# Kernel optimization log

Hardware: AMD Instinct MI355X
Metric: run time of the kernel (lower is better)

## Reference

```python
import jax, jax.numpy as jnp
import numpy as np

HEADS = 8
SR = 8


def _layernorm(x, g, b):
    m = jnp.mean(x, axis=-1, keepdims=True)
    v = jnp.var(x, axis=-1, keepdims=True)
    return (x - m) / jnp.sqrt(v + 1e-5) * g + b


def _sr_conv(x, w, b):
    # x: [B,C,H,W], w: [C,C,SR,SR] (OIHW), stride=SR, no padding
    y = jax.lax.conv_general_dilated(x, w, (SR, SR), 'VALID',
                                     dimension_numbers=('NCHW', 'OIHW', 'NCHW'))
    return y + b[None, :, None, None]


def _attn(xq, xkv, qw, kvw, pw, pb, srw, srb, lng, lnb, H, W):
    # xq: [B,N,C] queries (also residual); xkv: [B,N,C] key/value source
    B, N, C = xq.shape
    hd = C // HEADS
    scale = hd ** -0.5
    q = (xq @ qw.T).reshape(B, N, HEADS, hd).transpose(0, 2, 1, 3)  # [B,h,N,d]
    x_ = xkv.transpose(0, 2, 1).reshape(B, C, H, W)
    x_ = _sr_conv(x_, srw, srb).reshape(B, C, -1).transpose(0, 2, 1)  # [B,Nkv,C]
    x_ = _layernorm(x_, lng, lnb)
    kv = (x_ @ kvw.T).reshape(B, -1, 2, HEADS, hd).transpose(2, 0, 3, 1, 4)
    k, v = kv[0], kv[1]  # [B,h,Nkv,d]
    a = jax.nn.softmax(jnp.einsum('bhnd,bhmd->bhnm', q, k) * scale, axis=-1)
    o = jnp.einsum('bhnm,bhmd->bhnd', a, v).transpose(0, 2, 1, 3).reshape(B, N, C)
    return (o + xq) @ pw.T + pb


def _forward(x1, x2,
             sa1_qw, sa1_kvw, sa1_pw, sa1_pb, sa1_srw, sa1_srb, sa1_lng, sa1_lnb,
             ca12_qw, ca12_kvw, ca12_pw, ca12_pb, ca12_srw, ca12_srb, ca12_lng, ca12_lnb,
             sa2_qw, sa2_kvw, sa2_pw, sa2_pb, sa2_srw, sa2_srb, sa2_lng, sa2_lnb,
             ca21_qw, ca21_kvw, ca21_pw, ca21_pb, ca21_srw, ca21_srb, ca21_lng, ca21_lnb,
             pw, pb):
    B, C, H, W = x1.shape
    x1f = x1.reshape(B, C, H * W).transpose(0, 2, 1)
    x2f = x2.reshape(B, C, H * W).transpose(0, 2, 1)
    a = _attn(x1f, x1f, sa1_qw, sa1_kvw, sa1_pw, sa1_pb, sa1_srw, sa1_srb, sa1_lng, sa1_lnb, H, W)
    # CrossAttention(x2_flat, x1_self): queries/residual from x2, kv from x1_self
    b = _attn(x2f, a, ca12_qw, ca12_kvw, ca12_pw, ca12_pb, ca12_srw, ca12_srb, ca12_lng, ca12_lnb, H, W)
    c = _attn(b, b, sa2_qw, sa2_kvw, sa2_pw, sa2_pb, sa2_srw, sa2_srb, sa2_lng, sa2_lnb, H, W)
    d = _attn(a, c, ca21_qw, ca21_kvw, ca21_pw, ca21_pb, ca21_srw, ca21_srb, ca21_lng, ca21_lnb, H, W)
    fuse = d @ pw.T + pb
    return fuse.transpose(0, 2, 1).reshape(B, C, H, W)


def setup_inputs() -> dict:
    key = jax.random.key(0)
    B, C, H, W = 2, 64, 112, 112
    keys = iter(jax.random.split(key, 64))
    nrm = lambda shape, s=0.02: jax.random.normal(next(keys), shape, jnp.float32) * s
    d = {
        'x1': jax.random.normal(next(keys), (B, C, H, W), jnp.float32),
        'x2': jax.random.normal(next(keys), (B, C, H, W), jnp.float32),
    }
    conv_std = float(np.sqrt(2.0 / (SR * SR * C)))
    for p in ['sa1', 'ca12', 'sa2', 'ca21']:
        d[p + '_qw'] = nrm((C, C))
        d[p + '_kvw'] = nrm((2 * C, C))
        d[p + '_pw'] = nrm((C, C))
        d[p + '_pb'] = jnp.zeros((C,), jnp.float32)
        d[p + '_srw'] = nrm((C, C, SR, SR), conv_std)
        d[p + '_srb'] = jnp.zeros((C,), jnp.float32)
        d[p + '_lng'] = jnp.ones((C,), jnp.float32)
        d[p + '_lnb'] = jnp.zeros((C,), jnp.float32)
    d['pw'] = nrm((C, C))
    d['pb'] = jnp.zeros((C,), jnp.float32)
    return d


def reference(x1, x2,
              sa1_qw, sa1_kvw, sa1_pw, sa1_pb, sa1_srw, sa1_srb, sa1_lng, sa1_lnb,
              ca12_qw, ca12_kvw, ca12_pw, ca12_pb, ca12_srw, ca12_srb, ca12_lng, ca12_lnb,
              sa2_qw, sa2_kvw, sa2_pw, sa2_pb, sa2_srw, sa2_srb, sa2_lng, sa2_lnb,
              ca21_qw, ca21_kvw, ca21_pw, ca21_pb, ca21_srw, ca21_srb, ca21_lng, ca21_lnb,
              pw, pb):
    return _forward(x1, x2,
                    sa1_qw, sa1_kvw, sa1_pw, sa1_pb, sa1_srw, sa1_srb, sa1_lng, sa1_lnb,
                    ca12_qw, ca12_kvw, ca12_pw, ca12_pb, ca12_srw, ca12_srb, ca12_lng, ca12_lnb,
                    sa2_qw, sa2_kvw, sa2_pw, sa2_pb, sa2_srw, sa2_srb, sa2_lng, sa2_lnb,
                    ca21_qw, ca21_kvw, ca21_pw, ca21_pb, ca21_srw, ca21_srb, ca21_lng, ca21_lnb,
                    pw, pb)
```

## Files before the change

### kernel.cpp

```cpp
#include <hip/hip_runtime.h>
#include <hip/hip_bf16.h>

#define NPIX 12544
#define NKV 196
#define CCH 64

typedef _Float16 half2_t __attribute__((ext_vector_type(2)));
typedef _Float16 half4_t __attribute__((ext_vector_type(4)));
typedef float float4_t __attribute__((ext_vector_type(4)));
typedef __fp16 fp16v2_t __attribute__((ext_vector_type(2)));

#if defined(__has_builtin)
#if __has_builtin(__builtin_amdgcn_fdot2)
#define HAVE_FDOT2 1
#endif
#if __has_builtin(__builtin_amdgcn_cvt_pkrtz)
#define HAVE_PKRTZ 1
#endif
#if __has_builtin(__builtin_amdgcn_exp2f)
#define HAVE_EXP2 1
#endif
#if __has_builtin(__builtin_amdgcn_mfma_f32_16x16x16f16)
#define HAVE_MFMA16 1
#endif
#endif

__device__ __forceinline__ float dot2acc(half2_t a, half2_t b, float c) {
#ifdef HAVE_FDOT2
  return __builtin_amdgcn_fdot2(a, b, c, false);
#else
  return c + (float)a.x * (float)b.x + (float)a.y * (float)b.y;
#endif
}

__device__ __forceinline__ half2_t pack2(float a, float b) {
#ifdef HAVE_PKRTZ
  union { fp16v2_t r; half2_t h; } u;
  u.r = __builtin_amdgcn_cvt_pkrtz(a, b);
  return u.h;
#else
  half2_t v; v.x = (_Float16)a; v.y = (_Float16)b; return v;
#endif
}

__device__ __forceinline__ half2_t as_h2(uint u) {
  union { uint v; half2_t h; } c; c.v = u; return c.h;
}
__device__ __forceinline__ uint h2u(half2_t h) {
  union { half2_t h; uint v; } c; c.h = h; return c.v;
}
__device__ __forceinline__ float fexp2(float x) {
#ifdef HAVE_EXP2
  return __builtin_amdgcn_exp2f(x);
#else
  return exp2f(x);
#endif
}

__device__ __forceinline__ float4_t mfma16(half4_t a, half4_t b, float4_t c) {
#ifdef HAVE_MFMA16
  return __builtin_amdgcn_mfma_f32_16x16x16f16(a, b, c, 0, 0, 0);
#else
  asm volatile("v_mfma_f32_16x16x16_f16 %0, %1, %2, %0" : "+v"(c) : "v"(a), "v"(b));
  return c;
#endif
}

union U2H4 { uint2 u; half4_t h; };

#define QSCALE 0.5100974012336431f

__global__ __launch_bounds__(256) void k_prep(
    const float* __restrict__ x1, const float* __restrict__ x2,
    float* __restrict__ x1f, float* __restrict__ x2f,
    const float* __restrict__ s0, const float* __restrict__ s1,
    const float* __restrict__ s2, const float* __restrict__ s3,
    float* __restrict__ wt,
    const float* __restrict__ fpw, const float* __restrict__ fpb,
    const float* __restrict__ pw4, const float* __restrict__ pb4,
    const float* __restrict__ pw0, const float* __restrict__ pw1,
    const float* __restrict__ pw2,
    uint* __restrict__ pwh, float* __restrict__ pbc) {
  __shared__ float smem[2 * 64 * 65 + 64];
  int blk = blockIdx.x, t = threadIdx.x;
  float (*tile)[65] = (float(*)[65])smem;
  if (blk < 784) {
    int tensor = blk / 392; int rem = blk - tensor * 392;
    int b = rem / 196; int t64 = rem % 196; int n0 = t64 * 64;
    const float* src = tensor ? x2 : x1;
    float* dst = tensor ? x2f : x1f;
    for (int i = 0; i < 16; ++i) {
      int c = i * 4 + (t >> 6);
      int n = t & 63;
      tile[c][n] = src[(b * 64 + c) * NPIX + n0 + n];
    }
    __syncthreads();
    for (int i = 0; i < 16; ++i) {
      int n = i * 4 + (t >> 6);
      int c = t & 63;
      dst[(b * NPIX + n0 + n) * 64 + c] = tile[c][n];
    }
  } else if (blk < 1040) {
    int id = blk - 784; int a = id >> 6; int ci = id & 63;
    const float* s = (a == 0) ? s0 : (a == 1) ? s1 : (a == 2) ? s2 : s3;
    float* d = wt + a * 262144;
    for (int i = 0; i < 16; ++i) {
      int co = i * 4 + (t >> 6);
      int ij = t & 63;
      tile[co][ij] = s[co * 4096 + ci * 64 + ij];
    }
    __syncthreads();
    for (int i = 0; i < 16; ++i) {
      int ij = i * 4 + (t >> 6);
      int co = t & 63;
      d[(ij * 64 + ci) * 64 + co] = tile[co][ij];
    }
  } else if (blk == 1040) {
    float (*A)[65] = (float(*)[65])smem;
    float (*B)[65] = (float(*)[65])(smem + 4160);
    float* bb = smem + 8320;
    for (int i = 0; i < 16; ++i) {
      int idx = i * 256 + t;
      A[idx >> 6][idx & 63] = fpw[idx];
      B[idx >> 6][idx & 63] = pw4[idx];
    }
    if (t < 64) bb[t] = pb4[t];
    __syncthreads();
    int i = t >> 2, jq = t & 3;
    float acc[16];
#pragma unroll
    for (int jj = 0; jj < 16; ++jj) acc[jj] = 0.f;
    for (int k = 0; k < 64; ++k) {
      float a = A[i][k];
#pragma unroll
      for (int jj = 0; jj < 16; ++jj) acc[jj] += a * B[k][jq * 16 + jj];
    }
#pragma unroll
    for (int m = 0; m < 8; ++m)
      pwh[3 * 2048 + (jq * 8 + m) * 64 + i] = h2u(pack2(acc[2 * m], acc[2 * m + 1]));
    if (t < 64) {
      float s = fpb[t];
      for (int k = 0; k < 64; ++k) s += A[t][k] * bb[k];
      pbc[t] = s;
    }
  } else {
    int a = blk - 1041;
    const float* pw = (a == 0) ? pw0 : (a == 1) ? pw1 : pw2;
    for (int i = 0; i < 8; ++i) {
      int idx = i * 256 + t;
      int co = idx & 63, c2 = idx >> 6;
      float2 wv = *(const float2*)(pw + co * 64 + c2 * 2);
      pwh[a * 2048 + c2 * 64 + co] = h2u(pack2(wv.x, wv.y));
    }
  }
}

__global__ __launch_bounds__(256) void k_conv(
    const float* __restrict__ xf, const float* __restrict__ wt,
    float* __restrict__ part) {
  __shared__ __align__(16) float act[8 * 8 * 72];
  __shared__ float red[16][8][65];
  int g = blockIdx.x % 49, s = blockIdx.x / 49;
  int t = threadIdx.x;
  for (int q = 0; q < 5; ++q) {
    int fi = q * 256 + t;
    if (fi < 1152) {
      int row = fi / 18, pos = fi % 18;
      if (pos < 16) {
        int pix = row >> 3, ijl = row & 7;
        int ij = s * 8 + ijl, ii = ij >> 3, jj = ij & 7;
        int p = g * 8 + pix, b = p / 196, pi = p % 196;
        int py = pi / 14, px = pi % 14;
        *(float4*)&act[row * 72 + pos * 4] =
            *(const float4*)(xf + (size_t)(b * NPIX + (8 * py + ii) * 112 + 8 * px + jj) * 64 + pos * 4);
      }
    }
  }
  __syncthreads();
  int coq = t & 15, kp = t >> 4;
  int ijl = kp >> 1, ci0 = (kp & 1) * 32;
  float acc[8][4];
#pragma unroll
  for (int p = 0; p < 8; ++p)
#pragma unroll
    for (int c = 0; c < 4; ++c) acc[p][c] = 0.f;
  const float* wb = wt + ((s * 8 + ijl) * 64 + ci0) * 64 + coq * 4;
  const float* ab = act + ijl * 72 + ci0;
  for (int kk = 0; kk < 32; ++kk) {
    float4 w4 = *(const float4*)(wb + kk * 64);
#pragma unroll
    for (int p = 0; p < 8; ++p) {
      float a = ab[p * 576 + kk];
      acc[p][0] += a * w4.x; acc[p][1] += a * w4.y;
      acc[p][2] += a * w4.z; acc[p][3] += a * w4.w;
    }
  }
#pragma unroll
  for (int p = 0; p < 8; ++p)
#pragma unroll
    for (int c = 0; c < 4; ++c) red[kp][p][coq * 4 + c] = acc[p][c];
  __syncthreads();
  for (int q = 0; q < 2; ++q) {
    int oi = t + q * 256;
    int pix = oi >> 6, co = oi & 63;
    float sum = 0.f;
#pragma unroll
    for (int k = 0; k < 16; ++k) sum += red[k][pix][co];
    int p = g * 8 + pix;
    part[(s * 392 + p) * 64 + co] = sum;
  }
}

__global__ __launch_bounds__(128) void k_lnkv(
    const float* __restrict__ part, const float* __restrict__ srb,
    const float* __restrict__ lng, const float* __restrict__ lnb,
    const float* __restrict__ kvw,
    _Float16* __restrict__ kbuf, _Float16* __restrict__ vbuf) {
  __shared__ __align__(16) float yn[64];
  __shared__ __align__(16) float4 lkvw[16][128];
  int p = blockIdx.x, t = threadIdx.x;
  for (int i = 0; i < 64; ++i) {
    int idx = i * 128 + t;
    int co2 = idx >> 6, ci = idx & 63;
    ((float*)lkvw)[(ci >> 2) * 512 + co2 * 4 + (ci & 3)] = kvw[idx];
  }
  if (t < 64) {
    float y = 0.f;
    for (int s = 0; s < 8; ++s) y += part[(s * 392 + p) * 64 + t];
    y += srb[t];
    float s1 = y, s2 = y * y;
#pragma unroll
    for (int off = 32; off; off >>= 1) { s1 += __shfl_xor(s1, off); s2 += __shfl_xor(s2, off); }
    float mean = s1 * 0.015625f;
    float var = s2 * 0.015625f - mean * mean;
    float rs = rsqrtf(var + 1e-5f);
    yn[t] = (y - mean) * rs * lng[t] + lnb[t];
  }
  __syncthreads();
  float acc = 0.f;
#pragma unroll
  for (int c4 = 0; c4 < 16; ++c4) {
    float4 w4 = lkvw[c4][t];
    float4 y4 = *(const float4*)&yn[c4 * 4];
    acc += y4.x * w4.x + y4.y * w4.y + y4.z * w4.z + y4.w * w4.w;
  }
  int b = p / 196, pi = p % 196;
  int h = (t & 63) >> 3, d = t & 7;
  if (t < 64) kbuf[((b * 8 + h) * 196 + pi) * 8 + d] = (_Float16)acc;
  else        vbuf[((b * 8 + h) * 8 + d) * 196 + pi] = (_Float16)acc;
}

template <bool FINAL>
__global__ __launch_bounds__(512, 2) void k_score_out(
    const float* __restrict__ xqf, const float* __restrict__ qw,
    const _Float16* __restrict__ kbuf, const _Float16* __restrict__ vbuf,
    const uint* __restrict__ pwh, const float* __restrict__ pb,
    float* __restrict__ outp) {
  __shared__ __align__(16) uint sW[2048];
  __shared__ __align__(16) uint sX[64 * 33];
  __shared__ __align__(16) uint lq[8 * 64 * 4];
  __shared__ __align__(16) uint lo[64 * 34];
  int blk = blockIdx.x;
  int b = blk / 196, tileb = blk % 196;
  int t = threadIdx.x;
  int h = t >> 6, l = t & 63;
  int r15 = l & 15, g = l >> 4;
  for (int i = t; i < 2048; i += 512) {
    int co = i & 63, c2 = i >> 6;
    float2 wv = *(const float2*)(qw + co * 64 + c2 * 2);
    sW[c2 * 64 + co] = h2u(pack2(wv.x * QSCALE, wv.y * QSCALE));
  }
  for (int i = t; i < 2048; i += 512) {
    int rr = i >> 5, c2 = i & 31;
    float2 v = *(const float2*)(xqf + ((size_t)b * NPIX + (size_t)tileb * 64 + rr) * 64 + c2 * 2);
    sX[rr * 33 + c2] = h2u(pack2(v.x, v.y));
  }
  __syncthreads();
  {
    float q8[8];
#pragma unroll
    for (int j = 0; j < 8; ++j) q8[j] = 0.f;
#pragma unroll
    for (int c2 = 0; c2 < 32; ++c2) {
      half2_t xv = as_h2(sX[l * 33 + c2]);
      uint4 w0 = *(const uint4*)&sW[c2 * 64 + h * 8];
      uint4 w1 = *(const uint4*)&sW[c2 * 64 + h * 8 + 4];
      q8[0] = dot2acc(xv, as_h2(w0.x), q8[0]);
      q8[1] = dot2acc(xv, as_h2(w0.y), q8[1]);
      q8[2] = dot2acc(xv, as_h2(w0.z), q8[2]);
      q8[3] = dot2acc(xv, as_h2(w0.w), q8[3]);
      q8[4] = dot2acc(xv, as_h2(w1.x), q8[4]);
      q8[5] = dot2acc(xv, as_h2(w1.y), q8[5]);
      q8[6] = dot2acc(xv, as_h2(w1.z), q8[6]);
      q8[7] = dot2acc(xv, as_h2(w1.w), q8[7]);
    }
    uint4 qp;
    qp.x = h2u(pack2(q8[0], q8[1])); qp.y = h2u(pack2(q8[2], q8[3]));
    qp.z = h2u(pack2(q8[4], q8[5])); qp.w = h2u(pack2(q8[6], q8[7]));
    *(uint4*)&lq[(h * 64 + l) * 4] = qp;
  }
  __syncthreads();
  int bh = b * 8 + h;
  half4_t kf[13], vf[13];
#pragma unroll
  for (int tt = 0; tt < 13; ++tt) {
    int m = tt * 16 + r15;
    if (g < 2 && m < 196) {
      U2H4 u; u.u = *(const uint2*)(kbuf + ((size_t)bh * 196 + m) * 8 + 4 * g);
      kf[tt] = u.h;
    } else {
      kf[tt] = (half4_t)(_Float16)0.f;
    }
    int mv = tt * 16 + 4 * g;
    if (r15 < 8 && mv + 3 < 196) {
      U2H4 u; u.u = *(const uint2*)(vbuf + ((size_t)bh * 8 + r15) * 196 + mv);
      vf[tt] = u.h;
    } else {
      vf[tt] = (half4_t)(_Float16)0.f;
    }
  }
#pragma unroll 1
  for (int rt = 0; rt < 4; ++rt) {
    int rbase = rt * 16;
    half4_t qf;
    if (g < 2) {
      U2H4 u; u.u = *(const uint2*)((const _Float16*)nullptr);
      u.u = *(const uint2*)&lq[(h * 64 + rbase + r15) * 4 + 2 * g];
      qf = u.h;
    } else {
      qf = (half4_t)(_Float16)0.f;
    }
    float4_t sacc[13];
#pragma unroll
    for (int tt = 0; tt < 13; ++tt) {
      float4_t z = {0.f, 0.f, 0.f, 0.f};
      sacc[tt] = mfma16(kf[tt], qf, z);
    }
    float ssum = 0.f;
    half4_t pbf[13];
#pragma unroll
    for (int tt = 0; tt < 13; ++tt) {
      float e0, e1, e2, e3;
      if (tt == 12 && g > 0) {
        e0 = e1 = e2 = e3 = 0.f;
      } else {
        e0 = fexp2(sacc[tt][0]); e1 = fexp2(sacc[tt][1]);
        e2 = fexp2(sacc[tt][2]); e3 = fexp2(sacc[tt][3]);
      }
      ssum += (e0 + e1) + (e2 + e3);
      half2_t p01 = pack2(e0, e1), p23 = pack2(e2, e3);
      half4_t pv; pv.x = p01.x; pv.y = p01.y; pv.z = p23.x; pv.w = p23.y;
      pbf[tt] = pv;
    }
    ssum += __shfl_xor(ssum, 16);
    ssum += __shfl_xor(ssum, 32);
    float rl = 1.f / ssum;
    float4_t oacc = {0.f, 0.f, 0.f, 0.f};
#pragma unroll
    for (int tt = 0; tt < 13; ++tt) oacc = mfma16(vf[tt], pbf[tt], oacc);
    if (g < 2) {
      uint2 ov;
      ov.x = h2u(pack2(oacc[0] * rl, oacc[1] * rl));
      ov.y = h2u(pack2(oacc[2] * rl, oacc[3] * rl));
      *(uint2*)&lo[(rbase + r15) * 34 + h * 4 + 2 * g] = ov;
    }
  }
  __syncthreads();
  for (int i = t; i < 2048; i += 512) sW[i] = pwh[i];
  __syncthreads();
  int r2 = t >> 3, cq = t & 7;
  size_t gr2 = (size_t)b * NPIX + (size_t)tileb * 64 + r2;
  float acc[8];
#pragma unroll
  for (int k = 0; k < 8; ++k) acc[k] = pb[cq * 8 + k];
#pragma unroll
  for (int c2 = 0; c2 < 32; ++c2) {
    half2_t sv = as_h2(lo[r2 * 34 + c2]) + as_h2(sX[r2 * 33 + c2]);
    uint4 w0 = *(const uint4*)&sW[c2 * 64 + cq * 8];
    uint4 w1 = *(const uint4*)&sW[c2 * 64 + cq * 8 + 4];
    acc[0] = dot2acc(sv, as_h2(w0.x), acc[0]);
    acc[1] = dot2acc(sv, as_h2(w0.y), acc[1]);
    acc[2] = dot2acc(sv, as_h2(w0.z), acc[2]);
    acc[3] = dot2acc(sv, as_h2(w0.w), acc[3]);
    acc[4] = dot2acc(sv, as_h2(w1.x), acc[4]);
    acc[5] = dot2acc(sv, as_h2(w1.y), acc[5]);
    acc[6] = dot2acc(sv, as_h2(w1.z), acc[6]);
    acc[7] = dot2acc(sv, as_h2(w1.w), acc[7]);
  }
  if (!FINAL) {
    float4 v0, v1;
    v0.x = acc[0]; v0.y = acc[1]; v0.z = acc[2]; v0.w = acc[3];
    v1.x = acc[4]; v1.y = acc[5]; v1.z = acc[6]; v1.w = acc[7];
    float* orow = outp + gr2 * 64 + cq * 8;
    *(float4*)orow = v0;
    *(float4*)(orow + 4) = v1;
  } else {
    __syncthreads();
    uint2 p0, p1;
    p0.x = h2u(pack2(acc[0], acc[1])); p0.y = h2u(pack2(acc[2], acc[3]));
    p1.x = h2u(pack2(acc[4], acc[5])); p1.y = h2u(pack2(acc[6], acc[7]));
    *(uint2*)&lo[r2 * 34 + cq * 4] = p0;
    *(uint2*)&lo[r2 * 34 + cq * 4 + 2] = p1;
    __syncthreads();
    for (int i = t; i < 4096; i += 512) {
      int c = i >> 6, rr = i & 63;
      half2_t pr = as_h2(lo[rr * 34 + (c >> 1)]);
      float val = (c & 1) ? (float)pr.y : (float)pr.x;
      outp[((size_t)(b * 64 + c)) * NPIX + (size_t)tileb * 64 + rr] = val;
    }
  }
}

extern "C" void kernel_launch(void* const* d_in, const int* in_sizes, int n_in,
                              void* d_out, int out_size, void* d_ws, size_t ws_size,
                              hipStream_t stream) {
  const float* x1 = (const float*)d_in[0];
  const float* x2 = (const float*)d_in[1];
  const float *qw[4], *kvw[4], *pwv[4], *pbv[4], *srw[4], *srb[4], *lng[4], *lnb[4];
  for (int i = 0; i < 4; ++i) {
    const int base = 2 + i * 8;
    qw[i]  = (const float*)d_in[base + 0];
    kvw[i] = (const float*)d_in[base + 1];
    pwv[i] = (const float*)d_in[base + 2];
    pbv[i] = (const float*)d_in[base + 3];
    srw[i] = (const float*)d_in[base + 4];
    srb[i] = (const float*)d_in[base + 5];
    lng[i] = (const float*)d_in[base + 6];
    lnb[i] = (const float*)d_in[base + 7];
  }
  const float* fpw = (const float*)d_in[34];
  const float* fpb = (const float*)d_in[35];
  float* out = (float*)d_out;

  char* ws = (char*)d_ws;
  const size_t SZ = (size_t)2 * NPIX * 64 * 4;
  float* slot0 = (float*)(ws);
  float* slot1 = (float*)(ws + SZ);
  float* slot2 = (float*)(ws + 2 * SZ);
  size_t off = 3 * SZ;
  float* wt    = (float*)(ws + off); off += 4u * 1048576;
  float* part  = (float*)(ws + off); off += 802816;
  _Float16* kbuf = (_Float16*)(ws + off); off += 50176;
  _Float16* vbuf = (_Float16*)(ws + off); off += 50176;
  uint* pwh    = (uint*)(ws + off); off += 4 * 2048 * 4;
  float* pbc   = (float*)(ws + off); off += 256;

  float* xf1 = slot0; float* xf2 = slot1;
  float* abuf = slot2; float* bbuf = slot0; float* cbuf = slot1;

  k_prep<<<1044, 256, 0, stream>>>(x1, x2, xf1, xf2,
                                   srw[0], srw[1], srw[2], srw[3], wt,
                                   fpw, fpb, pwv[3], pbv[3],
                                   pwv[0], pwv[1], pwv[2], pwh, pbc);

  const float* xqs[4] = {xf1, xf2, bbuf, abuf};
  const float* kvs[4] = {xf1, abuf, bbuf, cbuf};
  float* outs[3]      = {abuf, bbuf, cbuf};
  for (int i = 0; i < 4; ++i) {
    k_conv<<<392, 256, 0, stream>>>(kvs[i], wt + i * 262144, part);
    k_lnkv<<<392, 128, 0, stream>>>(part, srb[i], lng[i], lnb[i], kvw[i], kbuf, vbuf);
    if (i < 3)
      k_score_out<false><<<392, 512, 0, stream>>>(xqs[i], qw[i], kbuf, vbuf,
                                                  pwh + i * 2048, pbv[i], outs[i]);
    else
      k_score_out<true><<<392, 512, 0, stream>>>(xqs[3], qw[3], kbuf, vbuf,
                                                 pwh + 3 * 2048, pbc, out);
  }
}
```

Baseline: 146.8 us.

## Fuse SR conv with LayerNorm+KV projection using fp16 packed weights

Merges the strided conv and the LayerNorm/KV-projection kernels into one kernel per output pixel, removing the partial-sum buffer and one launch per stage. The conv weights are pre-transposed into packed fp16 pairs and activations are converted to fp16 in shared memory, so the conv uses fdot2 instead of fp32 FMAs. Each block now streams the full 64x64x64 weight set itself (no split over kernel positions across blocks), which raises per-block global weight traffic and lowers precision of the conv inputs.

```diff
diff --git a/kernel.cpp b/kernel.cpp
--- a/kernel.cpp
+++ b/kernel.cpp
@@ -75,7 +75,7 @@
     float* __restrict__ x1f, float* __restrict__ x2f,
     const float* __restrict__ s0, const float* __restrict__ s1,
     const float* __restrict__ s2, const float* __restrict__ s3,
-    float* __restrict__ wt,
+    uint* __restrict__ wth,
     const float* __restrict__ fpw, const float* __restrict__ fpb,
     const float* __restrict__ pw4, const float* __restrict__ pb4,
     const float* __restrict__ pw0, const float* __restrict__ pw1,
@@ -101,19 +101,18 @@
       dst[(b * NPIX + n0 + n) * 64 + c] = tile[c][n];
     }
   } else if (blk < 1040) {
-    int id = blk - 784; int a = id >> 6; int ci = id & 63;
+    int id = blk - 784; int a = id >> 6; int co = id & 63;
     const float* s = (a == 0) ? s0 : (a == 1) ? s1 : (a == 2) ? s2 : s3;
-    float* d = wt + a * 262144;
-    for (int i = 0; i < 16; ++i) {
-      int co = i * 4 + (t >> 6);
-      int ij = t & 63;
-      tile[co][ij] = s[co * 4096 + ci * 64 + ij];
-    }
+    float* cw = smem;
+    for (int i = 0; i < 16; ++i)
+      cw[i * 256 + t] = s[co * 4096 + i * 256 + t];
     __syncthreads();
-    for (int i = 0; i < 16; ++i) {
-      int ij = i * 4 + (t >> 6);
-      int co = t & 63;
-      d[(ij * 64 + ci) * 64 + co] = tile[co][ij];
+    uint* wdst = wth + (size_t)a * 131072;
+    for (int q = 0; q < 8; ++q) {
+      int oi = q * 256 + t;
+      int ij = oi >> 5, ci2 = oi & 31;
+      wdst[((size_t)ij * 64 + co) * 32 + ci2] =
+          h2u(pack2(cw[(2 * ci2) * 64 + ij], cw[(2 * ci2 + 1) * 64 + ij]));
     }
   } else if (blk == 1040) {
     float (*A)[65] = (float(*)[65])smem;
@@ -155,78 +154,52 @@
   }
 }
 
-__global__ __launch_bounds__(256) void k_conv(
-    const float* __restrict__ xf, const float* __restrict__ wt,
-    float* __restrict__ part) {
-  __shared__ __align__(16) float act[8 * 8 * 72];
-  __shared__ float red[16][8][65];
-  int g = blockIdx.x % 49, s = blockIdx.x / 49;
-  int t = threadIdx.x;
-  for (int q = 0; q < 5; ++q) {
-    int fi = q * 256 + t;
-    if (fi < 1152) {
-      int row = fi / 18, pos = fi % 18;
-      if (pos < 16) {
-        int pix = row >> 3, ijl = row & 7;
-        int ij = s * 8 + ijl, ii = ij >> 3, jj = ij & 7;
-        int p = g * 8 + pix, b = p / 196, pi = p % 196;
-        int py = pi / 14, px = pi % 14;
-        *(float4*)&act[row * 72 + pos * 4] =
-            *(const float4*)(xf + (size_t)(b * NPIX + (8 * py + ii) * 112 + 8 * px + jj) * 64 + pos * 4);
-      }
-    }
-  }
-  __syncthreads();
-  int coq = t & 15, kp = t >> 4;
-  int ijl = kp >> 1, ci0 = (kp & 1) * 32;
-  float acc[8][4];
-#pragma unroll
-  for (int p = 0; p < 8; ++p)
-#pragma unroll
-    for (int c = 0; c < 4; ++c) acc[p][c] = 0.f;
-  const float* wb = wt + ((s * 8 + ijl) * 64 + ci0) * 64 + coq * 4;
-  const float* ab = act + ijl * 72 + ci0;
-  for (int kk = 0; kk < 32; ++kk) {
-    float4 w4 = *(const float4*)(wb + kk * 64);
-#pragma unroll
-    for (int p = 0; p < 8; ++p) {
-      float a = ab[p * 576 + kk];
-      acc[p][0] += a * w4.x; acc[p][1] += a * w4.y;
-      acc[p][2] += a * w4.z; acc[p][3] += a * w4.w;
-    }
-  }
-#pragma unroll
-  for (int p = 0; p < 8; ++p)
-#pragma unroll
-    for (int c = 0; c < 4; ++c) red[kp][p][coq * 4 + c] = acc[p][c];
-  __syncthreads();
+__global__ __launch_bounds__(512) void k_convlnkv(
+    const float* __restrict__ xf, const uint* __restrict__ wth,
+    const float* __restrict__ srb, const float* __restrict__ lng,
+    const float* __restrict__ lnb, const float* __restrict__ kvw,
+    _Float16* __restrict__ kbuf, _Float16* __restrict__ vbuf) {
+  __shared__ __align__(16) uint act16[64 * 32];
+  __shared__ float red[8][66];
+  __shared__ __align__(16) float yn[64];
+  __shared__ __align__(16) float lkvw[128 * 68];
+  int p = blockIdx.x, t = threadIdx.x;
+  int b = p / 196, pi = p % 196, py = pi / 14, px = pi % 14;
   for (int q = 0; q < 2; ++q) {
-    int oi = t + q * 256;
-    int pix = oi >> 6, co = oi & 63;
-    float sum = 0.f;
-#pragma unroll
-    for (int k = 0; k < 16; ++k) sum += red[k][pix][co];
-    int p = g * 8 + pix;
-    part[(s * 392 + p) * 64 + co] = sum;
-  }
-}
-
-__global__ __launch_bounds__(128) void k_lnkv(
-    const float* __restrict__ part, const float* __restrict__ srb,
-    const float* __restrict__ lng, const float* __restrict__ lnb,
-    const float* __restrict__ kvw,
-    _Float16* __restrict__ kbuf, _Float16* __restrict__ vbuf) {
-  __shared__ __align__(16) float yn[64];
-  __shared__ __align__(16) float4 lkvw[16][128];
-  int p = blockIdx.x, t = threadIdx.x;
-  for (int i = 0; i < 64; ++i) {
-    int idx = i * 128 + t;
-    int co2 = idx >> 6, ci = idx & 63;
-    ((float*)lkvw)[(ci >> 2) * 512 + co2 * 4 + (ci & 3)] = kvw[idx];
-  }
+    int fi = q * 512 + t;
+    int ij = fi >> 4, pos = fi & 15;
+    int ii = ij >> 3, jj = ij & 7;
+    float4 v = *(const float4*)(xf + ((size_t)(b * NPIX + (8 * py + ii) * 112 + 8 * px + jj) * 64 + pos * 4));
+    uint2 pk; pk.x = h2u(pack2(v.x, v.y)); pk.y = h2u(pack2(v.z, v.w));
+    *(uint2*)&act16[ij * 32 + pos * 2] = pk;
+  }
+  for (int i = 0; i < 16; ++i) {
+    int idx = i * 512 + t;
+    lkvw[(idx >> 6) * 68 + (idx & 63)] = kvw[idx];
+  }
+  __syncthreads();
+  int co = t & 63, g8 = t >> 6;
+  float acc = 0.f;
+  for (int ij8 = 0; ij8 < 8; ++ij8) {
+    int ij = g8 * 8 + ij8;
+    const uint4* wrow = (const uint4*)(wth + ((size_t)ij * 64 + co) * 32);
+    const uint4* arow = (const uint4*)(act16 + ij * 32);
+#pragma unroll
+    for (int u = 0; u < 8; ++u) {
+      uint4 w = wrow[u];
+      uint4 a = arow[u];
+      acc = dot2acc(as_h2(a.x), as_h2(w.x), acc);
+      acc = dot2acc(as_h2(a.y), as_h2(w.y), acc);
+      acc = dot2acc(as_h2(a.z), as_h2(w.z), acc);
+      acc = dot2acc(as_h2(a.w), as_h2(w.w), acc);
+    }
+  }
+  red[g8][co] = acc;
+  __syncthreads();
   if (t < 64) {
     float y = 0.f;
-    for (int s = 0; s < 8; ++s) y += part[(s * 392 + p) * 64 + t];
+#pragma unroll
+    for (int k = 0; k < 8; ++k) y += red[k][t];
     y += srb[t];
     float s1 = y, s2 = y * y;
 #pragma unroll
@@ -237,17 +210,23 @@
     yn[t] = (y - mean) * rs * lng[t] + lnb[t];
   }
   __syncthreads();
-  float acc = 0.f;
-#pragma unroll
-  for (int c4 = 0; c4 < 16; ++c4) {
-    float4 w4 = lkvw[c4][t];
-    float4 y4 = *(const float4*)&yn[c4 * 4];
-    acc += y4.x * w4.x + y4.y * w4.y + y4.z * w4.z + y4.w * w4.w;
-  }
-  int b = p / 196, pi = p % 196;
-  int h = (t & 63) >> 3, d = t & 7;
-  if (t < 64) kbuf[((b * 8 + h) * 196 + pi) * 8 + d] = (_Float16)acc;
-  else        vbuf[((b * 8 + h) * 8 + d) * 196 + pi] = (_Float16)acc;
+  if (t < 128) {
+    int o = t;
+    float a2 = 0.f;
+#pragma unroll
+    for (int c4 = 0; c4 < 16; ++c4) {
+      float4 w4 = *(const float4*)&lkvw[o * 68 + c4 * 4];
+      float4 y4 = *(const float4*)&yn[c4 * 4];
+      a2 += y4.x * w4.x + y4.y * w4.y + y4.z * w4.z + y4.w * w4.w;
+    }
+    if (o < 64) {
+      int h = o >> 3, d = o & 7;
+      kbuf[((b * 8 + h) * 196 + pi) * 8 + d] = (_Float16)a2;
+    } else {
+      int oo = o - 64, h = oo >> 3, d = oo & 7;
+      vbuf[((b * 8 + h) * 8 + d) * 196 + pi] = (_Float16)a2;
+    }
+  }
 }
 
 template <bool FINAL>
@@ -324,7 +303,7 @@
     int rbase = rt * 16;
     half4_t qf;
     if (g < 2) {
-      U2H4 u; u.u = *(const uint2*)((const _Float16*)nullptr);
+      U2H4 u;
       u.u = *(const uint2*)&lq[(h * 64 + rbase + r15) * 4 + 2 * g];
       qf = u.h;
     } else {
@@ -438,8 +417,7 @@
   float* slot1 = (float*)(ws + SZ);
   float* slot2 = (float*)(ws + 2 * SZ);
   size_t off = 3 * SZ;
-  float* wt    = (float*)(ws + off); off += 4u * 1048576;
-  float* part  = (float*)(ws + off); off += 802816;
+  uint* wth    = (uint*)(ws + off); off += (size_t)4 * 131072 * 4;
   _Float16* kbuf = (_Float16*)(ws + off); off += 50176;
   _Float16* vbuf = (_Float16*)(ws + off); off += 50176;
   uint* pwh    = (uint*)(ws + off); off += 4 * 2048 * 4;
@@ -449,7 +427,7 @@
   float* abuf = slot2; float* bbuf = slot0; float* cbuf = slot1;
 
   k_prep<<<1044, 256, 0, stream>>>(x1, x2, xf1, xf2,
-                                   srw[0], srw[1], srw[2], srw[3], wt,
+                                   srw[0], srw[1], srw[2], srw[3], wth,
                                    fpw, fpb, pwv[3], pbv[3],
                                    pwv[0], pwv[1], pwv[2], pwh, pbc);
 
@@ -457,8 +435,8 @@
   const float* kvs[4] = {xf1, abuf, bbuf, cbuf};
   float* outs[3]      = {abuf, bbuf, cbuf};
   for (int i = 0; i < 4; ++i) {
-    k_conv<<<392, 256, 0, stream>>>(kvs[i], wt + i * 262144, part);
-    k_lnkv<<<392, 128, 0, stream>>>(part, srb[i], lng[i], lnb[i], kvw[i], kbuf, vbuf);
+    k_convlnkv<<<392, 512, 0, stream>>>(kvs[i], wth + (size_t)i * 131072,
+                                        srb[i], lng[i], lnb[i], kvw[i], kbuf, vbuf);
     if (i < 3)
       k_score_out<false><<<392, 512, 0, stream>>>(xqs[i], qw[i], kbuf, vbuf,
                                                   pwh + i * 2048, pbv[i], outs[i]);
```

Measured after the change: 251.1 us. 71.0% more time.

## Halve row tile of score/output kernel to 32 rows and double grid size

Applied to the files above, without the earlier changes.

The fused attention-score/projection kernel now processes 32 query rows per block instead of 64, launching 784 blocks instead of 392 to fill more compute units on the 256-CU device. The Q projection splits the channel reduction across two half-waves and combines them with a cross-lane shuffle, and the output projection gives each thread 4 output channels instead of 8. The intent is better occupancy and load balance. The cost is that each block reloads the weight tiles and K/V fragments for half as many rows, doubling that redundant traffic.

```diff
diff --git a/kernel.cpp b/kernel.cpp
--- a/kernel.cpp
+++ b/kernel.cpp
@@ -257,11 +257,11 @@
     const uint* __restrict__ pwh, const float* __restrict__ pb,
     float* __restrict__ outp) {
   __shared__ __align__(16) uint sW[2048];
-  __shared__ __align__(16) uint sX[64 * 33];
-  __shared__ __align__(16) uint lq[8 * 64 * 4];
-  __shared__ __align__(16) uint lo[64 * 34];
+  __shared__ __align__(16) uint sX[32 * 33];
+  __shared__ __align__(16) uint lq[8 * 32 * 4];
+  __shared__ __align__(16) uint lo[32 * 34];
   int blk = blockIdx.x;
-  int b = blk / 196, tileb = blk % 196;
+  int b = blk / 392, tileb = blk % 392;
   int t = threadIdx.x;
   int h = t >> 6, l = t & 63;
   int r15 = l & 15, g = l >> 4;
@@ -270,19 +270,21 @@
     float2 wv = *(const float2*)(qw + co * 64 + c2 * 2);
     sW[c2 * 64 + co] = h2u(pack2(wv.x * QSCALE, wv.y * QSCALE));
   }
-  for (int i = t; i < 2048; i += 512) {
+  for (int i = t; i < 1024; i += 512) {
     int rr = i >> 5, c2 = i & 31;
-    float2 v = *(const float2*)(xqf + ((size_t)b * NPIX + (size_t)tileb * 64 + rr) * 64 + c2 * 2);
+    float2 v = *(const float2*)(xqf + ((size_t)b * NPIX + (size_t)tileb * 32 + rr) * 64 + c2 * 2);
     sX[rr * 33 + c2] = h2u(pack2(v.x, v.y));
   }
   __syncthreads();
   {
+    int r = l & 31, khalf = l >> 5;
     float q8[8];
 #pragma unroll
     for (int j = 0; j < 8; ++j) q8[j] = 0.f;
 #pragma unroll
-    for (int c2 = 0; c2 < 32; ++c2) {
-      half2_t xv = as_h2(sX[l * 33 + c2]);
+    for (int c2i = 0; c2i < 16; ++c2i) {
+      int c2 = khalf * 16 + c2i;
+      half2_t xv = as_h2(sX[r * 33 + c2]);
       uint4 w0 = *(const uint4*)&sW[c2 * 64 + h * 8];
       uint4 w1 = *(const uint4*)&sW[c2 * 64 + h * 8 + 4];
       q8[0] = dot2acc(xv, as_h2(w0.x), q8[0]);
@@ -294,10 +296,14 @@
       q8[6] = dot2acc(xv, as_h2(w1.z), q8[6]);
       q8[7] = dot2acc(xv, as_h2(w1.w), q8[7]);
     }
-    uint4 qp;
-    qp.x = h2u(pack2(q8[0], q8[1])); qp.y = h2u(pack2(q8[2], q8[3]));
-    qp.z = h2u(pack2(q8[4], q8[5])); qp.w = h2u(pack2(q8[6], q8[7]));
-    *(uint4*)&lq[(h * 64 + l) * 4] = qp;
+#pragma unroll
+    for (int j = 0; j < 8; ++j) q8[j] += __shfl_xor(q8[j], 32);
+    if (khalf == 0) {
+      uint4 qp;
+      qp.x = h2u(pack2(q8[0], q8[1])); qp.y = h2u(pack2(q8[2], q8[3]));
+      qp.z = h2u(pack2(q8[4], q8[5])); qp.w = h2u(pack2(q8[6], q8[7]));
+      *(uint4*)&lq[(h * 32 + r) * 4] = qp;
+    }
   }
   __syncthreads();
   int bh = b * 8 + h;
@@ -320,12 +326,12 @@
     }
   }
 #pragma unroll 1
-  for (int rt = 0; rt < 4; ++rt) {
+  for (int rt = 0; rt < 2; ++rt) {
     int rbase = rt * 16;
     half4_t qf;
     if (g < 2) {
-      U2H4 u; u.u = *(const uint2*)((const _Float16*)nullptr);
-      u.u = *(const uint2*)&lq[(h * 64 + rbase + r15) * 4 + 2 * g];
+      U2H4 u;
+      u.u = *(const uint2*)&lq[(h * 32 + rbase + r15) * 4 + 2 * g];
       qf = u.h;
     } else {
       qf = (half4_t)(_Float16)0.f;
@@ -368,45 +374,34 @@
   __syncthreads();
   for (int i = t; i < 2048; i += 512) sW[i] = pwh[i];
   __syncthreads();
-  int r2 = t >> 3, cq = t & 7;
-  size_t gr2 = (size_t)b * NPIX + (size_t)tileb * 64 + r2;
-  float acc[8];
-#pragma unroll
-  for (int k = 0; k < 8; ++k) acc[k] = pb[cq * 8 + k];
+  int r2 = t >> 4, cq = t & 15;
+  size_t gr2 = (size_t)b * NPIX + (size_t)tileb * 32 + r2;
+  float acc[4];
+#pragma unroll
+  for (int k = 0; k < 4; ++k) acc[k] = pb[cq * 4 + k];
 #pragma unroll
   for (int c2 = 0; c2 < 32; ++c2) {
     half2_t sv = as_h2(lo[r2 * 34 + c2]) + as_h2(sX[r2 * 33 + c2]);
-    uint4 w0 = *(const uint4*)&sW[c2 * 64 + cq * 8];
-    uint4 w1 = *(const uint4*)&sW[c2 * 64 + cq * 8 + 4];
-    acc[0] = dot2acc(sv, as_h2(w0.x), acc[0]);
-    acc[1] = dot2acc(sv, as_h2(w0.y), acc[1]);
-    acc[2] = dot2acc(sv, as_h2(w0.z), acc[2]);
-    acc[3] = dot2acc(sv, as_h2(w0.w), acc[3]);
-    acc[4] = dot2acc(sv, as_h2(w1.x), acc[4]);
-    acc[5] = dot2acc(sv, as_h2(w1.y), acc[5]);
-    acc[6] = dot2acc(sv, as_h2(w1.z), acc[6]);
-    acc[7] = dot2acc(sv, as_h2(w1.w), acc[7]);
+    uint4 w = *(const uint4*)&sW[c2 * 64 + cq * 4];
+    acc[0] = dot2acc(sv, as_h2(w.x), acc[0]);
+    acc[1] = dot2acc(sv, as_h2(w.y), acc[1]);
+    acc[2] = dot2acc(sv, as_h2(w.z), acc[2]);
+    acc[3] = dot2acc(sv, as_h2(w.w), acc[3]);
   }
   if (!FINAL) {
-    float4 v0, v1;
-    v0.x = acc[0]; v0.y = acc[1]; v0.z = acc[2]; v0.w = acc[3];
-    v1.x = acc[4]; v1.y = acc[5]; v1.z = acc[6]; v1.w = acc[7];
-    float* orow = outp + gr2 * 64 + cq * 8;
-    *(float4*)orow = v0;
-    *(float4*)(orow + 4) = v1;
+    float4 v;
+    v.x = acc[0]; v.y = acc[1]; v.z = acc[2]; v.w = acc[3];
+    *(float4*)(outp + gr2 * 64 + cq * 4) = v;
   } else {
     __syncthreads();
-    uint2 p0, p1;
-    p0.x = h2u(pack2(acc[0], acc[1])); p0.y = h2u(pack2(acc[2], acc[3]));
-    p1.x = h2u(pack2(acc[4], acc[5])); p1.y = h2u(pack2(acc[6], acc[7]));
-    *(uint2*)&lo[r2 * 34 + cq * 4] = p0;
-    *(uint2*)&lo[r2 * 34 + cq * 4 + 2] = p1;
+    lo[r2 * 34 + cq * 2] = h2u(pack2(acc[0], acc[1]));
+    lo[r2 * 34 + cq * 2 + 1] = h2u(pack2(acc[2], acc[3]));
     __syncthreads();
-    for (int i = t; i < 4096; i += 512) {
-      int c = i >> 6, rr = i & 63;
+    for (int i = t; i < 2048; i += 512) {
+      int c = i >> 5, rr = i & 31;
       half2_t pr = as_h2(lo[rr * 34 + (c >> 1)]);
       float val = (c & 1) ? (float)pr.y : (float)pr.x;
-      outp[((size_t)(b * 64 + c)) * NPIX + (size_t)tileb * 64 + rr] = val;
+      outp[((size_t)(b * 64 + c)) * NPIX + (size_t)tileb * 32 + rr] = val;
     }
   }
 }
@@ -460,10 +455,10 @@
     k_conv<<<392, 256, 0, stream>>>(kvs[i], wt + i * 262144, part);
     k_lnkv<<<392, 128, 0, stream>>>(part, srb[i], lng[i], lnb[i], kvw[i], kbuf, vbuf);
     if (i < 3)
-      k_score_out<false><<<392, 512, 0, stream>>>(xqs[i], qw[i], kbuf, vbuf,
+      k_score_out<false><<<784, 512, 0, stream>>>(xqs[i], qw[i], kbuf, vbuf,
                                                   pwh + i * 2048, pbv[i], outs[i]);
     else
-      k_score_out<true><<<392, 512, 0, stream>>>(xqs[3], qw[3], kbuf, vbuf,
+      k_score_out<true><<<784, 512, 0, stream>>>(xqs[3], qw[3], kbuf, vbuf,
                                                  pwh + 3 * 2048, pbc, out);
   }
 }
```

Measured after the change: 190.9 us. 30.0% more time.

## Compute Q projection with MFMA in-loop and preload projection weights early

Applied to the files above, without the earlier changes.

The per-thread fdot2 Q projection, which wrote to a shared `lq` buffer, is replaced by 16x16x16 MFMA ops computed per row tile inside the attention loop. Each wave-pair computes Q for 16 channels and uses a lane shuffle to hand the odd head its half. The output-projection weights are now loaded into an enlarged shared buffer at kernel start, which removes a later reload and barrier. This cuts ALU work and two syncs, at the cost of redundant MFMA work across paired waves, more shared memory for weights, and extra register pressure for the A fragments.

```diff
diff --git a/kernel.cpp b/kernel.cpp
--- a/kernel.cpp
+++ b/kernel.cpp
@@ -256,50 +256,36 @@
     const _Float16* __restrict__ kbuf, const _Float16* __restrict__ vbuf,
     const uint* __restrict__ pwh, const float* __restrict__ pb,
     float* __restrict__ outp) {
-  __shared__ __align__(16) uint sW[2048];
+  __shared__ __align__(16) uint sW[4096];
   __shared__ __align__(16) uint sX[64 * 33];
-  __shared__ __align__(16) uint lq[8 * 64 * 4];
   __shared__ __align__(16) uint lo[64 * 34];
   int blk = blockIdx.x;
   int b = blk / 196, tileb = blk % 196;
   int t = threadIdx.x;
   int h = t >> 6, l = t & 63;
   int r15 = l & 15, g = l >> 4;
+  int ht = h >> 1, odd = h & 1;
   for (int i = t; i < 2048; i += 512) {
     int co = i & 63, c2 = i >> 6;
     float2 wv = *(const float2*)(qw + co * 64 + c2 * 2);
     sW[c2 * 64 + co] = h2u(pack2(wv.x * QSCALE, wv.y * QSCALE));
   }
+  for (int i = t; i < 2048; i += 512) sW[2048 + i] = pwh[i];
   for (int i = t; i < 2048; i += 512) {
     int rr = i >> 5, c2 = i & 31;
     float2 v = *(const float2*)(xqf + ((size_t)b * NPIX + (size_t)tileb * 64 + rr) * 64 + c2 * 2);
     sX[rr * 33 + c2] = h2u(pack2(v.x, v.y));
   }
   __syncthreads();
-  {
-    float q8[8];
-#pragma unroll
-    for (int j = 0; j < 8; ++j) q8[j] = 0.f;
-#pragma unroll
-    for (int c2 = 0; c2 < 32; ++c2) {
-      half2_t xv = as_h2(sX[l * 33 + c2]);
-      uint4 w0 = *(const uint4*)&sW[c2 * 64 + h * 8];
-      uint4 w1 = *(const uint4*)&sW[c2 * 64 + h * 8 + 4];
-      q8[0] = dot2acc(xv, as_h2(w0.x), q8[0]);
-      q8[1] = dot2acc(xv, as_h2(w0.y), q8[1]);
-      q8[2] = dot2acc(xv, as_h2(w0.z), q8[2]);
-      q8[3] = dot2acc(xv, as_h2(w0.w), q8[3]);
-      q8[4] = dot2acc(xv, as_h2(w1.x), q8[4]);
-      q8[5] = dot2acc(xv, as_h2(w1.y), q8[5]);
-      q8[6] = dot2acc(xv, as_h2(w1.z), q8[6]);
-      q8[7] = dot2acc(xv, as_h2(w1.w), q8[7]);
-    }
-    uint4 qp;
-    qp.x = h2u(pack2(q8[0], q8[1])); qp.y = h2u(pack2(q8[2], q8[3]));
-    qp.z = h2u(pack2(q8[4], q8[5])); qp.w = h2u(pack2(q8[6], q8[7]));
-    *(uint4*)&lq[(h * 64 + l) * 4] = qp;
-  }
-  __syncthreads();
+  half4_t Aq[4];
+#pragma unroll
+  for (int ch = 0; ch < 4; ++ch) {
+    uint u0 = sW[(8 * ch + 2 * g) * 64 + ht * 16 + r15];
+    uint u1 = sW[(8 * ch + 2 * g + 1) * 64 + ht * 16 + r15];
+    half2_t a0 = as_h2(u0), a1 = as_h2(u1);
+    half4_t a; a.x = a0.x; a.y = a0.y; a.z = a1.x; a.w = a1.y;
+    Aq[ch] = a;
+  }
   int bh = b * 8 + h;
   half4_t kf[13], vf[13];
 #pragma unroll
@@ -322,11 +308,19 @@
 #pragma unroll 1
   for (int rt = 0; rt < 4; ++rt) {
     int rbase = rt * 16;
+    float4_t cq = {0.f, 0.f, 0.f, 0.f};
+#pragma unroll
+    for (int ch = 0; ch < 4; ++ch) {
+      U2H4 u; u.u = *(const uint2*)&sX[(rbase + r15) * 33 + 8 * ch + 2 * g];
+      cq = mfma16(Aq[ch], u.h, cq);
+    }
+    uint q0 = h2u(pack2(cq[0], cq[1]));
+    uint q1 = h2u(pack2(cq[2], cq[3]));
+    if (odd) { q0 = __shfl_xor(q0, 32); q1 = __shfl_xor(q1, 32); }
     half4_t qf;
     if (g < 2) {
-      U2H4 u; u.u = *(const uint2*)((const _Float16*)nullptr);
-      u.u = *(const uint2*)&lq[(h * 64 + rbase + r15) * 4 + 2 * g];
-      qf = u.h;
+      half2_t qa = as_h2(q0), qb = as_h2(q1);
+      qf.x = qa.x; qf.y = qa.y; qf.z = qb.x; qf.w = qb.y;
     } else {
       qf = (half4_t)(_Float16)0.f;
     }
@@ -366,8 +360,6 @@
     }
   }
   __syncthreads();
-  for (int i = t; i < 2048; i += 512) sW[i] = pwh[i];
-  __syncthreads();
   int r2 = t >> 3, cq = t & 7;
   size_t gr2 = (size_t)b * NPIX + (size_t)tileb * 64 + r2;
   float acc[8];
@@ -376,8 +368,8 @@
 #pragma unroll
   for (int c2 = 0; c2 < 32; ++c2) {
     half2_t sv = as_h2(lo[r2 * 34 + c2]) + as_h2(sX[r2 * 33 + c2]);
-    uint4 w0 = *(const uint4*)&sW[c2 * 64 + cq * 8];
-    uint4 w1 = *(const uint4*)&sW[c2 * 64 + cq * 8 + 4];
+    uint4 w0 = *(const uint4*)&sW[2048 + c2 * 64 + cq * 8];
+    uint4 w1 = *(const uint4*)&sW[2048 + c2 * 64 + cq * 8 + 4];
     acc[0] = dot2acc(sv, as_h2(w0.x), acc[0]);
     acc[1] = dot2acc(sv, as_h2(w0.y), acc[1]);
     acc[2] = dot2acc(sv, as_h2(w0.z), acc[2]);
```

Measured after the change: 152.8 us. 1.04x slower.
